# Optimization experiments

Measured on AMD Instinct MI355X. Metric: run time of the kernel, lower is better.

Reference implementation:

```python
import jax, jax.numpy as jnp
import numpy as np

N = 50000      # nodes
E = 800000     # edges (avg degree 16)
F_IN = 128     # in_channels
F_OUT = 64     # out_channels per head
H = 8          # attn heads
ALPHA = 0.2    # leaky relu slope


def setup_inputs() -> dict:
    key = jax.random.key(0)
    k1, k2, k3, k4, k5 = jax.random.split(key, 5)
    x = jax.random.normal(k1, (N, F_IN), dtype=jnp.float32)
    # guarantee every row appears as a source so rowsum > 0 (avoids NaN div)
    src = jnp.concatenate([jnp.arange(N, dtype=jnp.int32),
                           jax.random.randint(k2, (E - N,), 0, N, dtype=jnp.int32)])
    dst = jax.random.randint(k3, (E,), 0, N, dtype=jnp.int32)
    edge = jnp.stack([src, dst])  # [2, E]
    glorot = (6.0 / (F_IN + F_OUT)) ** 0.5
    W = jax.random.uniform(k4, (H, F_IN, F_OUT), jnp.float32, -glorot, glorot)
    a = jax.random.normal(k5, (H, 2 * F_OUT), dtype=jnp.float32) * 0.05
    return {"x": x, "edge": edge, "W": W, "a": a}


def reference(x, edge, W, a):
    # dropout p=0.6 treated in eval mode (identity); activation=None -> identity
    n = x.shape[0]
    src, dst = edge[0], edge[1]
    # per-head projected features: [H, N, F_OUT]
    h = jnp.einsum('nf,hfo->hno', x, W)
    a_src, a_dst = a[:, :F_OUT], a[:, F_OUT:]
    # edge scores a . cat(h_src, h_dst) decomposed into two node-level dots
    s = (jnp.einsum('hno,ho->hn', h, a_src)[:, src]
         + jnp.einsum('hno,ho->hn', h, a_dst)[:, dst])          # [H, E]
    edge_e = jnp.exp(-jax.nn.leaky_relu(s, ALPHA))               # [H, E]
    seg = lambda v: jax.ops.segment_sum(v, src, num_segments=n)
    rowsum = jax.vmap(seg)(edge_e)                               # [H, N] == spmm(e, ones)
    msg = edge_e[..., None] * h[:, dst, :]                       # [H, E, F_OUT]
    h_prime = jax.vmap(seg)(msg)                                 # [H, N, F_OUT]
    out = h_prime / rowsum[..., None]
    # concat heads: [N, H*F_OUT]
    return jnp.transpose(out, (1, 0, 2)).reshape(n, H * F_OUT)
```

## Files before the change

kernel.cpp:

```cpp
#include <hip/hip_runtime.h>
#include <hip/hip_bf16.h>
#include <math.h>

#define N_NODES 50000
#define N_EDGES 800000
#define FIN 128
#define FOUT 64
#define NH 8
#define ALPHA 0.2f
#define HSTRIDE (NH * FOUT)
#define SCAN_B 196

#define BPT_B  64
#define APERM_B 4
#define HIST_B 1563
#define PREP_B (BPT_B + APERM_B + HIST_B)

typedef __attribute__((ext_vector_type(8))) short bf16x8;
typedef __attribute__((ext_vector_type(4))) float f32x4;

__device__ __forceinline__ unsigned pack_bf2(float lo, float hi) {
    __hip_bfloat162 b = __float22bfloat162_rn(make_float2(lo, hi));
    return *(unsigned*)&b;
}

__global__ __launch_bounds__(256) void gat_prep(const float* __restrict__ W,
                                                const float* __restrict__ a,
                                                const int* __restrict__ src,
                                                unsigned* __restrict__ bpt,
                                                float* __restrict__ aperm,
                                                int* __restrict__ deg) {
    const int b = blockIdx.x;
    const int t = threadIdx.x;

    if (b < BPT_B) {
        const int gt   = b * 256 + t;
        const int dcol = gt >> 5;
        const int kq   = gt & 31;
        const int head = dcol & 7, col = dcol >> 3;
        const float* wp = W + (size_t)head * (FIN * FOUT) + (size_t)(kq * 4) * FOUT + col;
        uint2 pk;
        pk.x = pack_bf2(wp[0],        wp[FOUT]);
        pk.y = pack_bf2(wp[2 * FOUT], wp[3 * FOUT]);
        *(uint2*)(bpt + (size_t)dcol * (FIN / 2) + kq * 2) = pk;
    } else if (b < BPT_B + APERM_B) {
        const int idx  = (b - BPT_B) * 256 + t;
        const int tab  = idx >> 9;
        const int dcol = idx & 511;
        aperm[idx] = a[(dcol & 7) * (2 * FOUT) + tab * FOUT + (dcol >> 3)];
    } else {
        const int e = ((b - BPT_B - APERM_B) * 256 + t) * 2;
        if (e + 1 < N_EDGES) {
            const int2 s2 = *(const int2*)(src + e);
            atomicAdd(&deg[s2.x], 1);
            atomicAdd(&deg[s2.y], 1);
        } else if (e < N_EDGES) {
            atomicAdd(&deg[src[e]], 1);
        }
    }
}

__global__ __launch_bounds__(256) void gat_proj(const float* __restrict__ x,
                                                const unsigned short* __restrict__ bpt,
                                                const float* __restrict__ aperm,
                                                unsigned short* __restrict__ h2,
                                                float* __restrict__ ssrc,
                                                float* __restrict__ sdst) {
    const int lane = threadIdx.x & 63;
    const int wid  = blockIdx.x * 4 + (threadIdx.x >> 6);
    const int m0   = wid * 32;
    const int l15  = lane & 15;
    const int g    = lane >> 4;

    bf16x8 xf[2][4];
#pragma unroll
    for (int nh = 0; nh < 2; ++nh) {
        int node = m0 + nh * 16 + l15;
        if (node > N_NODES - 1) node = N_NODES - 1;
        const float* p = x + (size_t)node * FIN + g * 8;
#pragma unroll
        for (int ks = 0; ks < 4; ++ks) {
            const float4 a0 = *(const float4*)(p + ks * 32);
            const float4 a1 = *(const float4*)(p + ks * 32 + 4);
            unsigned* u = (unsigned*)&xf[nh][ks];
            u[0] = pack_bf2(a0.x, a0.y);
            u[1] = pack_bf2(a0.z, a0.w);
            u[2] = pack_bf2(a1.x, a1.y);
            u[3] = pack_bf2(a1.z, a1.w);
        }
    }

    float sc1[2][4], sc2[2][4];
#pragma unroll
    for (int nh = 0; nh < 2; ++nh)
#pragma unroll
        for (int r = 0; r < 4; ++r) { sc1[nh][r] = 0.f; sc2[nh][r] = 0.f; }

    for (int stp = 0; stp < 16; ++stp) {
        const int dc0 = stp * 32;
        f32x4 acc[2][2];
#pragma unroll
        for (int dh = 0; dh < 2; ++dh)
#pragma unroll
            for (int nh = 0; nh < 2; ++nh)
                acc[dh][nh] = (f32x4){0.f, 0.f, 0.f, 0.f};

#pragma unroll
        for (int dh = 0; dh < 2; ++dh) {
            const unsigned short* p = bpt + (size_t)(dc0 + dh * 16 + l15) * FIN + g * 8;
#pragma unroll
            for (int ks = 0; ks < 4; ++ks) {
                const bf16x8 af = *(const bf16x8*)(p + ks * 32);
                acc[dh][0] = __builtin_amdgcn_mfma_f32_16x16x32_bf16(af, xf[0][ks], acc[dh][0], 0, 0, 0);
                acc[dh][1] = __builtin_amdgcn_mfma_f32_16x16x32_bf16(af, xf[1][ks], acc[dh][1], 0, 0, 0);
            }
        }

#pragma unroll
        for (int dh = 0; dh < 2; ++dh) {
            const float4 ap1 = *(const float4*)&aperm[dc0 + dh * 16 + g * 4];
            const float4 ap2 = *(const float4*)&aperm[512 + dc0 + dh * 16 + g * 4];
#pragma unroll
            for (int nh = 0; nh < 2; ++nh) {
                sc1[nh][0] += acc[dh][nh][0] * ap1.x;  sc2[nh][0] += acc[dh][nh][0] * ap2.x;
                sc1[nh][1] += acc[dh][nh][1] * ap1.y;  sc2[nh][1] += acc[dh][nh][1] * ap2.y;
                sc1[nh][2] += acc[dh][nh][2] * ap1.z;  sc2[nh][2] += acc[dh][nh][2] * ap2.z;
                sc1[nh][3] += acc[dh][nh][3] * ap1.w;  sc2[nh][3] += acc[dh][nh][3] * ap2.w;
            }
        }

#pragma unroll
        for (int nh = 0; nh < 2; ++nh) {
            const int node = m0 + nh * 16 + l15;
            if (node < N_NODES) {
#pragma unroll
                for (int dh = 0; dh < 2; ++dh) {
                    const int dc = dc0 + dh * 16 + g * 4;
                    uint2 pk;
                    pk.x = pack_bf2(acc[dh][nh][0], acc[dh][nh][1]);
                    pk.y = pack_bf2(acc[dh][nh][2], acc[dh][nh][3]);
                    *(uint2*)((char*)h2 + ((size_t)node * HSTRIDE + dc) * 2) = pk;
                }
            }
        }
    }

#pragma unroll
    for (int nh = 0; nh < 2; ++nh) {
        const int node = m0 + nh * 16 + l15;
        float4 v1 = make_float4(sc1[nh][0], sc1[nh][1], sc1[nh][2], sc1[nh][3]);
        float4 v2 = make_float4(sc2[nh][0], sc2[nh][1], sc2[nh][2], sc2[nh][3]);
        v1.x += __shfl_xor(v1.x, 32, 64); v1.y += __shfl_xor(v1.y, 32, 64);
        v1.z += __shfl_xor(v1.z, 32, 64); v1.w += __shfl_xor(v1.w, 32, 64);
        v2.x += __shfl_xor(v2.x, 32, 64); v2.y += __shfl_xor(v2.y, 32, 64);
        v2.z += __shfl_xor(v2.z, 32, 64); v2.w += __shfl_xor(v2.w, 32, 64);
        if (node < N_NODES) {
            if (g == 0) { *(float4*)&ssrc[node * 8]     = v1; *(float4*)&sdst[node * 8]     = v2; }
            if (g == 1) { *(float4*)&ssrc[node * 8 + 4] = v1; *(float4*)&sdst[node * 8 + 4] = v2; }
        }
    }
}

__global__ __launch_bounds__(256) void scan_bsum(const int* __restrict__ deg,
                                                 int* __restrict__ bsum) {
    __shared__ int sm[256];
    const int t   = threadIdx.x;
    const int gid = blockIdx.x * 256 + t;
    sm[t] = (gid < N_NODES) ? deg[gid] : 0;
    __syncthreads();
#pragma unroll
    for (int off = 128; off > 0; off >>= 1) {
        if (t < off) sm[t] += sm[t + off];
        __syncthreads();
    }
    if (t == 0) bsum[blockIdx.x] = sm[0];
}

__global__ __launch_bounds__(256) void scan_write(const int* __restrict__ deg,
                                                  const int* __restrict__ bsum,
                                                  int* __restrict__ row_start,
                                                  int* __restrict__ cursor) {
    __shared__ int smp[256];
    __shared__ int sm[256];
    const int t = threadIdx.x;
    const int b = blockIdx.x;

    const int pv = (t < SCAN_B) ? bsum[t] : 0;
    smp[t] = pv;
    __syncthreads();
    for (int off = 1; off < 256; off <<= 1) {
        const int u = (t >= off) ? smp[t - off] : 0;
        __syncthreads();
        smp[t] += u;
        __syncthreads();
    }
    const int base = (b > 0) ? smp[b - 1] : 0;

    const int gid = b * 256 + t;
    const int v   = (gid < N_NODES) ? deg[gid] : 0;
    sm[t] = v;
    __syncthreads();
    for (int off = 1; off < 256; off <<= 1) {
        const int u = (t >= off) ? sm[t - off] : 0;
        __syncthreads();
        sm[t] += u;
        __syncthreads();
    }
    if (gid < N_NODES) {
        const int rs = base + sm[t] - v;
        row_start[gid] = rs;
        cursor[gid]    = rs;
    }
    if (b == 0 && t == 0) row_start[N_NODES] = N_EDGES;
}

__global__ __launch_bounds__(256) void gat_fill(const int* __restrict__ src,
                                                const int* __restrict__ dst,
                                                int* __restrict__ cursor,
                                                int* __restrict__ csr_dst) {
    const int e = blockIdx.x * 256 + threadIdx.x;
    if (e >= N_EDGES) return;
    const int pos = atomicAdd(&cursor[src[e]], 1);
    csr_dst[pos] = dst[e];
}

#define GAT_LD(KK) (*(const uint4*)(h2b + ((size_t)(unsigned)__builtin_amdgcn_readlane(d, (KK)) << 10) + lofs))

#define GAT_FMA(HV, KK) do {                                                          \
    const float e0 = __int_as_float(__builtin_amdgcn_readlane(__float_as_int(e[0]), (KK))); \
    const float e1 = __int_as_float(__builtin_amdgcn_readlane(__float_as_int(e[1]), (KK))); \
    const float e2 = __int_as_float(__builtin_amdgcn_readlane(__float_as_int(e[2]), (KK))); \
    const float e3 = __int_as_float(__builtin_amdgcn_readlane(__float_as_int(e[3]), (KK))); \
    const float e4 = __int_as_float(__builtin_amdgcn_readlane(__float_as_int(e[4]), (KK))); \
    const float e5 = __int_as_float(__builtin_amdgcn_readlane(__float_as_int(e[5]), (KK))); \
    const float e6 = __int_as_float(__builtin_amdgcn_readlane(__float_as_int(e[6]), (KK))); \
    const float e7 = __int_as_float(__builtin_amdgcn_readlane(__float_as_int(e[7]), (KK))); \
    acc[0] += e0 * __int_as_float((HV).x << 16);                                      \
    acc[1] += e1 * __int_as_float((HV).x & 0xFFFF0000u);                              \
    acc[2] += e2 * __int_as_float((HV).y << 16);                                      \
    acc[3] += e3 * __int_as_float((HV).y & 0xFFFF0000u);                              \
    acc[4] += e4 * __int_as_float((HV).z << 16);                                      \
    acc[5] += e5 * __int_as_float((HV).z & 0xFFFF0000u);                              \
    acc[6] += e6 * __int_as_float((HV).w << 16);                                      \
    acc[7] += e7 * __int_as_float((HV).w & 0xFFFF0000u);                              \
} while (0)

__global__ __launch_bounds__(256) void gat_gather(const int* __restrict__ row_start,
                                                  const int* __restrict__ csr_dst,
                                                  const __hip_bfloat16* __restrict__ h2,
                                                  const float* __restrict__ ssrc,
                                                  const float* __restrict__ sdst,
                                                  float* __restrict__ out) {
    const int n    = (int)((blockIdx.x * 256 + threadIdx.x) >> 6);
    const int lane = threadIdx.x & 63;
    if (n >= N_NODES) return;

    const int start = row_start[n];
    const int degn  = row_start[n + 1] - start;

    const float4 sa = *(const float4*)(ssrc + n * 8);
    const float4 sb = *(const float4*)(ssrc + n * 8 + 4);
    const float s0[8] = {sa.x, sa.y, sa.z, sa.w, sb.x, sb.y, sb.z, sb.w};

    float acc[8] = {0.f, 0.f, 0.f, 0.f, 0.f, 0.f, 0.f, 0.f};
    float rs[8]  = {0.f, 0.f, 0.f, 0.f, 0.f, 0.f, 0.f, 0.f};
    const unsigned lofs = (unsigned)lane * 16u;
    const char* h2b = (const char*)h2;

    for (int base = 0; base < degn; base += 64) {
        const int j      = base + lane;
        const bool valid = j < degn;
        const int d = valid ? __builtin_nontemporal_load(csr_dst + start + j) : 0;
        float4 qa = make_float4(0.f, 0.f, 0.f, 0.f), qb = qa;
        if (valid) {
            qa = *(const float4*)(sdst + d * 8);
            qb = *(const float4*)(sdst + d * 8 + 4);
        }
        const float q[8] = {qa.x, qa.y, qa.z, qa.w, qb.x, qb.y, qb.z, qb.w};
        float e[8];
#pragma unroll
        for (int i = 0; i < 8; ++i) {
            const float sv = s0[i] + q[i];
            const float lr = sv > 0.f ? sv : ALPHA * sv;
            e[i] = valid ? __expf(-lr) : 0.f;
            rs[i] += e[i];
        }

        const int cnt = min(64, degn - base);
        int k = 0;
        if (cnt >= 8) {
            uint4 q0 = GAT_LD(0), q1 = GAT_LD(1), q2 = GAT_LD(2), q3 = GAT_LD(3);
            for (k = 0; k + 8 <= cnt; k += 4) {
                GAT_FMA(q0, k + 0); q0 = GAT_LD(k + 4);
                GAT_FMA(q1, k + 1); q1 = GAT_LD(k + 5);
                GAT_FMA(q2, k + 2); q2 = GAT_LD(k + 6);
                GAT_FMA(q3, k + 3); q3 = GAT_LD(k + 7);
            }
            GAT_FMA(q0, k + 0);
            GAT_FMA(q1, k + 1);
            GAT_FMA(q2, k + 2);
            GAT_FMA(q3, k + 3);
            k += 4;
        }
        for (; k < cnt; ++k) {
            const uint4 qv = GAT_LD(k);
            GAT_FMA(qv, k);
        }
    }

#pragma unroll
    for (int i = 0; i < 8; ++i)
#pragma unroll
        for (int m = 1; m < 64; m <<= 1) rs[i] += __shfl_xor(rs[i], m, 64);

#pragma unroll
    for (int i = 0; i < 8; ++i)
        __builtin_nontemporal_store(acc[i] / rs[i], &out[(size_t)n * HSTRIDE + i * 64 + lane]);
}

extern "C" void kernel_launch(void* const* d_in, const int* in_sizes, int n_in,
                              void* d_out, int out_size, void* d_ws, size_t ws_size,
                              hipStream_t stream) {
    const float* x    = (const float*)d_in[0];
    const int*   edge = (const int*)d_in[1];
    const float* W    = (const float*)d_in[2];
    const float* a    = (const float*)d_in[3];
    float*       out  = (float*)d_out;

    char* ws = (char*)d_ws;
    size_t off = 0;
    unsigned short* h2  = (unsigned short*)(ws + off); off += (size_t)N_NODES * HSTRIDE * 2;
    unsigned short* bpt = (unsigned short*)(ws + off); off += (size_t)HSTRIDE * FIN * 2;
    float* aperm  = (float*)(ws + off); off += (size_t)2 * HSTRIDE * sizeof(float);
    float* ssrc   = (float*)(ws + off); off += (size_t)N_NODES * NH * sizeof(float);
    float* sdst   = (float*)(ws + off); off += (size_t)N_NODES * NH * sizeof(float);
    int*   row_st = (int*)  (ws + off); off += (size_t)(N_NODES + 4) * sizeof(int);
    int*   cursor = (int*)  (ws + off); off += (size_t)N_NODES * sizeof(int);
    int*   deg    = (int*)  (ws + off); off += (size_t)N_NODES * sizeof(int);
    int*   bsum   = (int*)  (ws + off); off += (size_t)256 * sizeof(int);
    int*   csrd   = (int*)  (ws + off); off += (size_t)N_EDGES * sizeof(int);

    const int* srcv = edge;
    const int* dstv = edge + N_EDGES;

    hipMemsetAsync(deg, 0, (size_t)N_NODES * sizeof(int), stream);

    gat_prep  <<<PREP_B, 256, 0, stream>>>(W, a, srcv, (unsigned*)bpt, aperm, deg);
    scan_bsum <<<SCAN_B, 256, 0, stream>>>(deg, bsum);
    scan_write<<<SCAN_B, 256, 0, stream>>>(deg, bsum, row_st, cursor);
    gat_fill  <<<(N_EDGES + 255) / 256, 256, 0, stream>>>(srcv, dstv, cursor, csrd);
    gat_proj  <<<(N_NODES + 127) / 128, 256, 0, stream>>>(x, bpt, aperm, h2, ssrc, sdst);
    gat_gather<<<(N_NODES + 3) / 4, 256, 0, stream>>>(row_st, csrd, (const __hip_bfloat16*)h2, ssrc, sdst, out);
}
```

Before: 266.6 us.

## Degree-sort gather order, fuse fill with projection, use packed f32x2 FMAs

Builds a histogram of node degrees during the block scan and emits a node order sorted by descending degree, which the gather kernel then follows so heavy rows are scheduled first and wave load imbalance drops. The CSR fill and the projection kernels are merged into one launch, saving a launch and letting the two run concurrently. The gather accumulators become f32x2 vectors so the compiler can emit packed FMAs. The cost is extra atomics and an indirection through the order array, plus scattered output writes.

```diff
diff --git a/kernel.cpp b/kernel.cpp
--- a/kernel.cpp
+++ b/kernel.cpp
@@ -16,12 +16,23 @@
 #define HIST_B 1563
 #define PREP_B (BPT_B + APERM_B + HIST_B)
 
+#define FILL_B 3125
+#define PROJ_B 391
+
 typedef __attribute__((ext_vector_type(8))) short bf16x8;
 typedef __attribute__((ext_vector_type(4))) float f32x4;
+typedef __attribute__((ext_vector_type(2))) float f32x2;
 
 __device__ __forceinline__ unsigned pack_bf2(float lo, float hi) {
     __hip_bfloat162 b = __float22bfloat162_rn(make_float2(lo, hi));
     return *(unsigned*)&b;
+}
+
+__device__ __forceinline__ f32x2 bf2f2(unsigned u) {
+    f32x2 r;
+    r.x = __int_as_float(u << 16);
+    r.y = __int_as_float(u & 0xFFFF0000u);
+    return r;
 }
 
 __global__ __launch_bounds__(256) void gat_prep(const float* __restrict__ W,
@@ -60,14 +71,99 @@
     }
 }
 
-__global__ __launch_bounds__(256) void gat_proj(const float* __restrict__ x,
-                                                const unsigned short* __restrict__ bpt,
-                                                const float* __restrict__ aperm,
-                                                unsigned short* __restrict__ h2,
-                                                float* __restrict__ ssrc,
-                                                float* __restrict__ sdst) {
+__global__ __launch_bounds__(256) void scan_bsum(const int* __restrict__ deg,
+                                                 int* __restrict__ bsum,
+                                                 int* __restrict__ dbin) {
+    __shared__ int sm[256];
+    __shared__ int lbin[128];
+    const int t   = threadIdx.x;
+    const int gid = blockIdx.x * 256 + t;
+    if (t < 128) lbin[t] = 0;
+    const int v = (gid < N_NODES) ? deg[gid] : 0;
+    sm[t] = v;
+    __syncthreads();
+    if (gid < N_NODES) atomicAdd(&lbin[127 - min(v, 127)], 1);
+#pragma unroll
+    for (int off = 128; off > 0; off >>= 1) {
+        if (t < off) sm[t] += sm[t + off];
+        __syncthreads();
+    }
+    if (t == 0) bsum[blockIdx.x] = sm[0];
+    if (t < 128 && lbin[t]) atomicAdd(&dbin[t], lbin[t]);
+}
+
+__global__ __launch_bounds__(256) void scan_write(const int* __restrict__ deg,
+                                                  const int* __restrict__ bsum,
+                                                  const int* __restrict__ dbin,
+                                                  int* __restrict__ bincur,
+                                                  int* __restrict__ row_start,
+                                                  int* __restrict__ cursor,
+                                                  int* __restrict__ order) {
+    __shared__ int smp[256];
+    __shared__ int sm[256];
+    __shared__ int sbin[128];
+    __shared__ int sbex[128];
+    const int t = threadIdx.x;
+    const int b = blockIdx.x;
+
+    const int pv   = (t < SCAN_B) ? bsum[t] : 0;
+    const int obin = (t < 128) ? dbin[t] : 0;
+    smp[t] = pv;
+    if (t < 128) sbin[t] = obin;
+    __syncthreads();
+    for (int off = 1; off < 256; off <<= 1) {
+        const int u  = (t >= off) ? smp[t - off] : 0;
+        const int ub = (t < 128 && t >= off) ? sbin[t - off] : 0;
+        __syncthreads();
+        smp[t] += u;
+        if (t < 128) sbin[t] += ub;
+        __syncthreads();
+    }
+    if (t < 128) sbex[t] = sbin[t] - obin;
+    const int base = (b > 0) ? smp[b - 1] : 0;
+
+    const int gid = b * 256 + t;
+    const int v   = (gid < N_NODES) ? deg[gid] : 0;
+    sm[t] = v;
+    __syncthreads();
+    for (int off = 1; off < 256; off <<= 1) {
+        const int u = (t >= off) ? sm[t - off] : 0;
+        __syncthreads();
+        sm[t] += u;
+        __syncthreads();
+    }
+    if (gid < N_NODES) {
+        const int rs = base + sm[t] - v;
+        row_start[gid] = rs;
+        cursor[gid]    = rs;
+        const int bin = 127 - min(v, 127);
+        const int pos = sbex[bin] + atomicAdd(&bincur[bin], 1);
+        order[pos] = gid;
+    }
+    if (b == 0 && t == 0) row_start[N_NODES] = N_EDGES;
+}
+
+__global__ __launch_bounds__(256) void gat_fillproj(const int* __restrict__ src,
+                                                    const int* __restrict__ dst,
+                                                    int* __restrict__ cursor,
+                                                    int* __restrict__ csr_dst,
+                                                    const float* __restrict__ x,
+                                                    const unsigned short* __restrict__ bpt,
+                                                    const float* __restrict__ aperm,
+                                                    unsigned short* __restrict__ h2,
+                                                    float* __restrict__ ssrc,
+                                                    float* __restrict__ sdst) {
+    if (blockIdx.x < FILL_B) {
+        const int e = blockIdx.x * 256 + threadIdx.x;
+        if (e < N_EDGES) {
+            const int pos = atomicAdd(&cursor[src[e]], 1);
+            csr_dst[pos] = dst[e];
+        }
+        return;
+    }
+
     const int lane = threadIdx.x & 63;
-    const int wid  = blockIdx.x * 4 + (threadIdx.x >> 6);
+    const int wid  = (blockIdx.x - FILL_B) * 4 + (threadIdx.x >> 6);
     const int m0   = wid * 32;
     const int l15  = lane & 15;
     const int g    = lane >> 4;
@@ -161,88 +257,22 @@
     }
 }
 
-__global__ __launch_bounds__(256) void scan_bsum(const int* __restrict__ deg,
-                                                 int* __restrict__ bsum) {
-    __shared__ int sm[256];
-    const int t   = threadIdx.x;
-    const int gid = blockIdx.x * 256 + t;
-    sm[t] = (gid < N_NODES) ? deg[gid] : 0;
-    __syncthreads();
-#pragma unroll
-    for (int off = 128; off > 0; off >>= 1) {
-        if (t < off) sm[t] += sm[t + off];
-        __syncthreads();
-    }
-    if (t == 0) bsum[blockIdx.x] = sm[0];
-}
-
-__global__ __launch_bounds__(256) void scan_write(const int* __restrict__ deg,
-                                                  const int* __restrict__ bsum,
-                                                  int* __restrict__ row_start,
-                                                  int* __restrict__ cursor) {
-    __shared__ int smp[256];
-    __shared__ int sm[256];
-    const int t = threadIdx.x;
-    const int b = blockIdx.x;
-
-    const int pv = (t < SCAN_B) ? bsum[t] : 0;
-    smp[t] = pv;
-    __syncthreads();
-    for (int off = 1; off < 256; off <<= 1) {
-        const int u = (t >= off) ? smp[t - off] : 0;
-        __syncthreads();
-        smp[t] += u;
-        __syncthreads();
-    }
-    const int base = (b > 0) ? smp[b - 1] : 0;
-
-    const int gid = b * 256 + t;
-    const int v   = (gid < N_NODES) ? deg[gid] : 0;
-    sm[t] = v;
-    __syncthreads();
-    for (int off = 1; off < 256; off <<= 1) {
-        const int u = (t >= off) ? sm[t - off] : 0;
-        __syncthreads();
-        sm[t] += u;
-        __syncthreads();
-    }
-    if (gid < N_NODES) {
-        const int rs = base + sm[t] - v;
-        row_start[gid] = rs;
-        cursor[gid]    = rs;
-    }
-    if (b == 0 && t == 0) row_start[N_NODES] = N_EDGES;
-}
-
-__global__ __launch_bounds__(256) void gat_fill(const int* __restrict__ src,
-                                                const int* __restrict__ dst,
-                                                int* __restrict__ cursor,
-                                                int* __restrict__ csr_dst) {
-    const int e = blockIdx.x * 256 + threadIdx.x;
-    if (e >= N_EDGES) return;
-    const int pos = atomicAdd(&cursor[src[e]], 1);
-    csr_dst[pos] = dst[e];
-}
-
 #define GAT_LD(KK) (*(const uint4*)(h2b + ((size_t)(unsigned)__builtin_amdgcn_readlane(d, (KK)) << 10) + lofs))
 
-#define GAT_FMA(HV, KK) do {                                                          \
-    const float e0 = __int_as_float(__builtin_amdgcn_readlane(__float_as_int(e[0]), (KK))); \
-    const float e1 = __int_as_float(__builtin_amdgcn_readlane(__float_as_int(e[1]), (KK))); \
-    const float e2 = __int_as_float(__builtin_amdgcn_readlane(__float_as_int(e[2]), (KK))); \
-    const float e3 = __int_as_float(__builtin_amdgcn_readlane(__float_as_int(e[3]), (KK))); \
-    const float e4 = __int_as_float(__builtin_amdgcn_readlane(__float_as_int(e[4]), (KK))); \
-    const float e5 = __int_as_float(__builtin_amdgcn_readlane(__float_as_int(e[5]), (KK))); \
-    const float e6 = __int_as_float(__builtin_amdgcn_readlane(__float_as_int(e[6]), (KK))); \
-    const float e7 = __int_as_float(__builtin_amdgcn_readlane(__float_as_int(e[7]), (KK))); \
-    acc[0] += e0 * __int_as_float((HV).x << 16);                                      \
-    acc[1] += e1 * __int_as_float((HV).x & 0xFFFF0000u);                              \
-    acc[2] += e2 * __int_as_float((HV).y << 16);                                      \
-    acc[3] += e3 * __int_as_float((HV).y & 0xFFFF0000u);                              \
-    acc[4] += e4 * __int_as_float((HV).z << 16);                                      \
-    acc[5] += e5 * __int_as_float((HV).z & 0xFFFF0000u);                              \
-    acc[6] += e6 * __int_as_float((HV).w << 16);                                      \
-    acc[7] += e7 * __int_as_float((HV).w & 0xFFFF0000u);                              \
+#define GAT_FMA(HV, KK) do {                                                                \
+    f32x2 ev;                                                                               \
+    ev.x = __int_as_float(__builtin_amdgcn_readlane(__float_as_int(e[0]), (KK)));           \
+    ev.y = __int_as_float(__builtin_amdgcn_readlane(__float_as_int(e[1]), (KK)));           \
+    acc2[0] += ev * bf2f2((HV).x);                                                          \
+    ev.x = __int_as_float(__builtin_amdgcn_readlane(__float_as_int(e[2]), (KK)));           \
+    ev.y = __int_as_float(__builtin_amdgcn_readlane(__float_as_int(e[3]), (KK)));           \
+    acc2[1] += ev * bf2f2((HV).y);                                                          \
+    ev.x = __int_as_float(__builtin_amdgcn_readlane(__float_as_int(e[4]), (KK)));           \
+    ev.y = __int_as_float(__builtin_amdgcn_readlane(__float_as_int(e[5]), (KK)));           \
+    acc2[2] += ev * bf2f2((HV).z);                                                          \
+    ev.x = __int_as_float(__builtin_amdgcn_readlane(__float_as_int(e[6]), (KK)));           \
+    ev.y = __int_as_float(__builtin_amdgcn_readlane(__float_as_int(e[7]), (KK)));           \
+    acc2[3] += ev * bf2f2((HV).w);                                                          \
 } while (0)
 
 __global__ __launch_bounds__(256) void gat_gather(const int* __restrict__ row_start,
@@ -250,10 +280,12 @@
                                                   const __hip_bfloat16* __restrict__ h2,
                                                   const float* __restrict__ ssrc,
                                                   const float* __restrict__ sdst,
+                                                  const int* __restrict__ order,
                                                   float* __restrict__ out) {
-    const int n    = (int)((blockIdx.x * 256 + threadIdx.x) >> 6);
+    const int wid  = (int)((blockIdx.x * 256 + threadIdx.x) >> 6);
     const int lane = threadIdx.x & 63;
-    if (n >= N_NODES) return;
+    if (wid >= N_NODES) return;
+    const int n = order[wid];
 
     const int start = row_start[n];
     const int degn  = row_start[n + 1] - start;
@@ -262,8 +294,10 @@
     const float4 sb = *(const float4*)(ssrc + n * 8 + 4);
     const float s0[8] = {sa.x, sa.y, sa.z, sa.w, sb.x, sb.y, sb.z, sb.w};
 
-    float acc[8] = {0.f, 0.f, 0.f, 0.f, 0.f, 0.f, 0.f, 0.f};
-    float rs[8]  = {0.f, 0.f, 0.f, 0.f, 0.f, 0.f, 0.f, 0.f};
+    f32x2 acc2[4];
+#pragma unroll
+    for (int i = 0; i < 4; ++i) acc2[i] = (f32x2){0.f, 0.f};
+    float rs[8] = {0.f, 0.f, 0.f, 0.f, 0.f, 0.f, 0.f, 0.f};
     const unsigned lofs = (unsigned)lane * 16u;
     const char* h2b = (const char*)h2;
 
@@ -314,8 +348,10 @@
         for (int m = 1; m < 64; m <<= 1) rs[i] += __shfl_xor(rs[i], m, 64);
 
 #pragma unroll
-    for (int i = 0; i < 8; ++i)
-        __builtin_nontemporal_store(acc[i] / rs[i], &out[(size_t)n * HSTRIDE + i * 64 + lane]);
+    for (int i = 0; i < 8; ++i) {
+        const float av = (i & 1) ? acc2[i >> 1].y : acc2[i >> 1].x;
+        __builtin_nontemporal_store(av / rs[i], &out[(size_t)n * HSTRIDE + i * 64 + lane]);
+    }
 }
 
 extern "C" void kernel_launch(void* const* d_in, const int* in_sizes, int n_in,
@@ -337,18 +373,22 @@
     int*   row_st = (int*)  (ws + off); off += (size_t)(N_NODES + 4) * sizeof(int);
     int*   cursor = (int*)  (ws + off); off += (size_t)N_NODES * sizeof(int);
     int*   deg    = (int*)  (ws + off); off += (size_t)N_NODES * sizeof(int);
+    int*   dbin   = (int*)  (ws + off); off += (size_t)128 * sizeof(int);
+    int*   bincur = (int*)  (ws + off); off += (size_t)128 * sizeof(int);
     int*   bsum   = (int*)  (ws + off); off += (size_t)256 * sizeof(int);
+    int*   order  = (int*)  (ws + off); off += (size_t)N_NODES * sizeof(int);
     int*   csrd   = (int*)  (ws + off); off += (size_t)N_EDGES * sizeof(int);
 
     const int* srcv = edge;
     const int* dstv = edge + N_EDGES;
 
-    hipMemsetAsync(deg, 0, (size_t)N_NODES * sizeof(int), stream);
-
-    gat_prep  <<<PREP_B, 256, 0, stream>>>(W, a, srcv, (unsigned*)bpt, aperm, deg);
-    scan_bsum <<<SCAN_B, 256, 0, stream>>>(deg, bsum);
-    scan_write<<<SCAN_B, 256, 0, stream>>>(deg, bsum, row_st, cursor);
-    gat_fill  <<<(N_EDGES + 255) / 256, 256, 0, stream>>>(srcv, dstv, cursor, csrd);
-    gat_proj  <<<(N_NODES + 127) / 128, 256, 0, stream>>>(x, bpt, aperm, h2, ssrc, sdst);
-    gat_gather<<<(N_NODES + 3) / 4, 256, 0, stream>>>(row_st, csrd, (const __hip_bfloat16*)h2, ssrc, sdst, out);
-}
+    hipMemsetAsync(deg, 0, ((size_t)N_NODES + 256) * sizeof(int), stream);
+
+    gat_prep    <<<PREP_B, 256, 0, stream>>>(W, a, srcv, (unsigned*)bpt, aperm, deg);
+    scan_bsum   <<<SCAN_B, 256, 0, stream>>>(deg, bsum, dbin);
+    scan_write  <<<SCAN_B, 256, 0, stream>>>(deg, bsum, dbin, bincur, row_st, cursor, order);
+    gat_fillproj<<<FILL_B + PROJ_B, 256, 0, stream>>>(srcv, dstv, cursor, csrd,
+                                                      x, bpt, aperm, h2, ssrc, sdst);
+    gat_gather  <<<(N_NODES + 3) / 4, 256, 0, stream>>>(row_st, csrd, (const __hip_bfloat16*)h2,
+                                                        ssrc, sdst, order, out);
+}
```

Measured after the change: 460.9 us. +72.9%, slower.
